# Kernel tuning notes

Hardware: AMD Instinct MI355X
Metric: run time of the kernel (lower is better)

Reference implementation:

```python
import jax, jax.numpy as jnp
import numpy as np

B, E, H, W = 8, 1024, 16, 1024
DH = E // H


def setup_inputs() -> dict:
    key = jax.random.key(0)
    ks = jax.random.split(key, 5)
    scale = E ** (-0.5)
    return {
        "x": jax.random.normal(ks[0], (3, B, E, W), dtype=jnp.float32),
        "L_Q": jax.random.normal(ks[1], (E, E), dtype=jnp.float32) * scale,
        "L_K": jax.random.normal(ks[2], (E, E), dtype=jnp.float32) * scale,
        "L_V": jax.random.normal(ks[3], (E, E), dtype=jnp.float32) * scale,
        "dense_M": jax.random.normal(ks[4], (E, E), dtype=jnp.float32) * scale,
        "dense_b": jnp.zeros((E, 1), dtype=jnp.float32),
    }


def reference(x, L_Q, L_K, L_V, dense_M, dense_b):
    # x: [3, B, E, W], channels-first sequences (dropout layers are identity in eval)
    K, Q, V = x[0], x[1], x[2]                      # each [B, E, W]
    K = jnp.einsum('ef,bfw->bew', L_K, K)
    Q = jnp.einsum('ef,bfw->bew', L_Q, Q)
    V = jnp.einsum('ef,bfw->bew', L_V, V)
    Kv = K.reshape(B, H, DH, W)
    Qv = Q.reshape(B, H, DH, W)
    Vv = V.reshape(B, H, DH, W)
    # Q_v^T @ K_v -> [B, H, Wq, Wk]
    scores = jnp.einsum('bhdq,bhdk->bhqk', Qv, Kv)
    # causal_factor = tril(-inf, diag=-1): -inf strictly below the diagonal (q > k)
    qi = jnp.arange(W)[:, None]
    ki = jnp.arange(W)[None, :]
    scores = jnp.where(qi > ki, -jnp.inf, scores)
    # softmax over the QUERY axis (-2), post-scaled by E^-0.5 (non-standard)
    attn = jax.nn.softmax(scores, axis=-2) * (E ** (-0.5))
    # V_v @ scores: contract over the query axis -> [B, H, DH, Wk]
    out = jnp.einsum('bhdq,bhqk->bhdk', Vv, attn).reshape(B, E, W)
    # dense output projection: M @ out + b (bias broadcasts over W)
    return jnp.einsum('ef,bfw->bew', dense_M, out) + dense_b
```

## Files before the change

### kernel.cpp

```cpp
#include <hip/hip_runtime.h>

typedef float  f4  __attribute__((ext_vector_type(4)));
typedef short  s8v __attribute__((ext_vector_type(8)));
typedef unsigned short u16;
typedef u16 us4 __attribute__((ext_vector_type(4)));

constexpr int En  = 1024;
constexpr int Wn  = 1024;
constexpr int Bn  = 8;
constexpr int Hn  = 16;
constexpr int DHn = 64;

__device__ inline u16 bf16rn(float x) {
    unsigned u = __float_as_uint(x);
    return (u16)((u + 0x7FFFu + ((u >> 16) & 1u)) >> 16);
}
__device__ inline float bf16tof(u16 h) { return __uint_as_float(((unsigned)h) << 16); }

#define GLD_LDS16(gp, lp) __builtin_amdgcn_global_load_lds(                      \
    (const __attribute__((address_space(1))) void*)(gp),                         \
    (__attribute__((address_space(3))) void*)(lp), 16, 0, 0)

__global__ void split_plain(const float* __restrict__ in, u16* __restrict__ hi,
                            u16* __restrict__ lo, int n4) {
    int i = blockIdx.x * blockDim.x + threadIdx.x;
    if (i >= n4) return;
    f4 v = ((const f4*)in)[i];
    us4 h, l;
    #pragma unroll
    for (int k = 0; k < 4; ++k) {
        u16 hh = bf16rn(v[k]);
        h[k] = hh;
        l[k] = bf16rn(v[k] - bf16tof(hh));
    }
    ((us4*)hi)[i] = h;
    ((us4*)lo)[i] = l;
}

__global__ void f32_to_bf16(const float* __restrict__ in, u16* __restrict__ out,
                            int n4) {
    int i = blockIdx.x * blockDim.x + threadIdx.x;
    if (i >= n4) return;
    f4 v = ((const f4*)in)[i];
    us4 o;
    #pragma unroll
    for (int k = 0; k < 4; ++k) o[k] = bf16rn(v[k]);
    ((us4*)out)[i] = o;
}

__global__ __launch_bounds__(256)
void split_t(const float* __restrict__ in, u16* __restrict__ hi,
             u16* __restrict__ lo) {
    __shared__ float T[32][33];
    const int z = blockIdx.z;
    const size_t zo = (size_t)z * En * Wn;
    const int r0 = blockIdx.y * 32, c0 = blockIdx.x * 32;
    const int t = threadIdx.x;
    const int row = t >> 3, c4 = (t & 7) << 2;

    f4 v = *(const f4*)&in[zo + (size_t)(r0 + row) * Wn + c0 + c4];
    T[row][c4 + 0] = v[0]; T[row][c4 + 1] = v[1];
    T[row][c4 + 2] = v[2]; T[row][c4 + 3] = v[3];
    __syncthreads();

    const int oc = row, r4 = c4;
    us4 h, l;
    #pragma unroll
    for (int i = 0; i < 4; ++i) {
        float x = T[r4 + i][oc];
        u16 hh = bf16rn(x);
        h[i] = hh;
        l[i] = bf16rn(x - bf16tof(hh));
    }
    *(us4*)&hi[zo + (size_t)(c0 + oc) * En + r0 + r4] = h;
    *(us4*)&lo[zo + (size_t)(c0 + oc) * En + r0 + r4] = l;
}

__global__ __launch_bounds__(256)
void qk_repack(const float* __restrict__ in, u16* __restrict__ oh,
               u16* __restrict__ ol) {
    __shared__ float T[64][65];
    const int bh = blockIdx.y, w0 = blockIdx.x * 64;
    const int t = threadIdx.x;
    const int row = t >> 2, cc = (t & 3) << 4;

    #pragma unroll
    for (int c = 0; c < 4; ++c) {
        f4 v = *(const f4*)&in[(size_t)(bh * 64 + row) * Wn + w0 + cc + c * 4];
        T[row][cc + c * 4 + 0] = v[0]; T[row][cc + c * 4 + 1] = v[1];
        T[row][cc + c * 4 + 2] = v[2]; T[row][cc + c * 4 + 3] = v[3];
    }
    __syncthreads();

    const size_t ob = ((size_t)bh * Wn + w0 + row) * 64 + cc;
    #pragma unroll
    for (int c = 0; c < 4; ++c) {
        us4 h, l;
        #pragma unroll
        for (int j = 0; j < 4; ++j) {
            float x = T[cc + c * 4 + j][row];
            u16 hh = bf16rn(x);
            h[j] = hh;
            l[j] = bf16rn(x - bf16tof(hh));
        }
        *(us4*)&oh[ob + c * 4] = h;
        *(us4*)&ol[ob + c * 4] = l;
    }
}

__global__ __launch_bounds__(256, 2)
void gemm_mfma(const u16* __restrict__ Ah,  const u16* __restrict__ Al,
               const u16* __restrict__ Bth, const u16* __restrict__ Btl,
               float* __restrict__ Y, const float* __restrict__ bias) {
    __shared__ u16 AsH[4096], AsL[4096], BsH[4096], BsL[4096];

    const int z  = blockIdx.z;
    const size_t zB = (size_t)z * Wn * En;
    const size_t zY = (size_t)z * En * Wn;
    const int e0 = blockIdx.y * 128, n0 = blockIdx.x * 128;
    const int t = threadIdx.x, lane = t & 63, wave = t >> 6;
    const int q = lane >> 4, r = lane & 15;
    const int m_off = (wave & 1) * 64, n_off = (wave >> 1) * 64;

    f4 acc[4][4];
    #pragma unroll
    for (int i = 0; i < 4; ++i)
        #pragma unroll
        for (int j = 0; j < 4; ++j) { acc[i][j][0]=0; acc[i][j][1]=0; acc[i][j][2]=0; acc[i][j][3]=0; }

    for (int kb = 0; kb < En; kb += 32) {
        __syncthreads();
        #pragma unroll
        for (int it = 0; it < 2; ++it) {
            const int id = t + 256 * it;
            const int u = id >> 3;
            const int p = (id & 7) ^ (u & 7);
            const int m = 2 * u + (p >> 2), g = p & 3;
            const size_t colA = (size_t)kb + 8 * g;
            const u16* ga_h = Ah  + (size_t)(e0 + m) * En + colA;
            const u16* ga_l = Al  + (size_t)(e0 + m) * En + colA;
            const u16* gb_h = Bth + zB + (size_t)(n0 + m) * En + colA;
            const u16* gb_l = Btl + zB + (size_t)(n0 + m) * En + colA;
            GLD_LDS16(ga_h, &AsH[id * 8]);
            GLD_LDS16(ga_l, &AsL[id * 8]);
            GLD_LDS16(gb_h, &BsH[id * 8]);
            GLD_LDS16(gb_l, &BsL[id * 8]);
        }
        __syncthreads();

        s8v aH[4], aL[4], bH[4], bL[4];
        #pragma unroll
        for (int i = 0; i < 4; ++i) {
            const int Ra = m_off + 16 * i + r;
            const int Rb = n_off + 16 * i + r;
            const int sa = ((((Ra & 1) << 2) | q) ^ ((Ra >> 1) & 7));
            const int sb = ((((Rb & 1) << 2) | q) ^ ((Rb >> 1) & 7));
            const int ai = ((Ra >> 1) * 8 + sa) * 8;
            const int bi = ((Rb >> 1) * 8 + sb) * 8;
            aH[i] = *(const s8v*)&AsH[ai];
            aL[i] = *(const s8v*)&AsL[ai];
            bH[i] = *(const s8v*)&BsH[bi];
            bL[i] = *(const s8v*)&BsL[bi];
        }
        #pragma unroll
        for (int i = 0; i < 4; ++i)
            #pragma unroll
            for (int j = 0; j < 4; ++j) {
                acc[i][j] = __builtin_amdgcn_mfma_f32_16x16x32_bf16(aH[i], bH[j], acc[i][j], 0, 0, 0);
                acc[i][j] = __builtin_amdgcn_mfma_f32_16x16x32_bf16(aH[i], bL[j], acc[i][j], 0, 0, 0);
                acc[i][j] = __builtin_amdgcn_mfma_f32_16x16x32_bf16(aL[i], bH[j], acc[i][j], 0, 0, 0);
            }
    }

    #pragma unroll
    for (int i = 0; i < 4; ++i) {
        #pragma unroll
        for (int reg = 0; reg < 4; ++reg) {
            const int e = e0 + m_off + 16 * i + q * 4 + reg;
            const float bv = bias ? bias[e] : 0.0f;
            #pragma unroll
            for (int j = 0; j < 4; ++j) {
                const int w = n0 + n_off + 16 * j + r;
                Y[zY + (size_t)e * Wn + w] = acc[i][j][reg] + bv;
            }
        }
    }
}

__global__ __launch_bounds__(256, 2)
void attn_mfma2(const u16* __restrict__ QTh, const u16* __restrict__ QTl,
                const u16* __restrict__ KTh, const u16* __restrict__ KTl,
                const u16* __restrict__ Vb,  float* __restrict__ Ao) {
    __shared__ u16 QsH[2][4096], QsL[2][4096], Vs[2][4096];
    __shared__ u16 PT[4][16][72];

    const int id   = blockIdx.x;
    const int rest = id >> 3;
    const int kb   = 15 - (rest & 15);
    const int bh   = (id & 7) + 8 * (rest >> 4);

    const int t = threadIdx.x, lane = t & 63, wave = t >> 6;
    const int r = lane & 15, quad = lane >> 4;
    const int k0 = kb * 64;
    const int kcol = k0 + wave * 16 + r;
    u16 (*pt)[72] = PT[wave];

    const size_t qkb = (size_t)bh * Wn * 64;
    const size_t vbb = (size_t)bh * 64 * Wn;

    s8v kH[2], kL[2];
    #pragma unroll
    for (int s = 0; s < 2; ++s) {
        const size_t a = qkb + (size_t)kcol * 64 + s * 32 + quad * 8;
        kH[s] = *(const s8v*)&KTh[a];
        kL[s] = *(const s8v*)&KTl[a];
    }

    f4 o[4];
    #pragma unroll
    for (int i = 0; i < 4; ++i) { o[i][0]=0; o[i][1]=0; o[i][2]=0; o[i][3]=0; }
    float m = -1e30f, l = 0.0f;

    auto stage = [&](int q0, int buf) {
        const size_t g = qkb + (size_t)q0 * 64;
        #pragma unroll
        for (int it = 0; it < 2; ++it) {
            const int c = t + it * 256;
            const int row = c >> 3;
            const int p   = (c & 7) ^ (row & 7);
            GLD_LDS16(QTh + g + (size_t)row * 64 + p * 8, &QsH[buf][c * 8]);
            GLD_LDS16(QTl + g + (size_t)row * 64 + p * 8, &QsL[buf][c * 8]);
            GLD_LDS16(Vb + vbb + (size_t)row * Wn + q0 + p * 8,
                      &Vs[buf][c * 8]);
        }
    };

    stage(0, 0);
    int buf = 0;

    for (int q0 = 0; q0 <= k0; q0 += 64) {
        __syncthreads();
        if (q0 + 64 <= k0) stage(q0 + 64, buf ^ 1);

        f4 sacc[4];
        #pragma unroll
        for (int mt = 0; mt < 4; ++mt) { sacc[mt][0]=0; sacc[mt][1]=0; sacc[mt][2]=0; sacc[mt][3]=0; }
        #pragma unroll
        for (int s = 0; s < 2; ++s) {
            const int sw = (((s * 4 + quad) ^ (r & 7)) << 3);
            #pragma unroll
            for (int mt = 0; mt < 4; ++mt) {
                const int a = (16 * mt + r) * 64 + sw;
                s8v qh = *(const s8v*)&QsH[buf][a];
                s8v ql = *(const s8v*)&QsL[buf][a];
                sacc[mt] = __builtin_amdgcn_mfma_f32_16x16x32_bf16(qh, kH[s], sacc[mt], 0, 0, 0);
                sacc[mt] = __builtin_amdgcn_mfma_f32_16x16x32_bf16(qh, kL[s], sacc[mt], 0, 0, 0);
                sacc[mt] = __builtin_amdgcn_mfma_f32_16x16x32_bf16(ql, kH[s], sacc[mt], 0, 0, 0);
            }
        }
        if (q0 == k0) {
            const int klocal = wave * 16 + r;
            #pragma unroll
            for (int mt = 0; mt < 4; ++mt)
                #pragma unroll
                for (int reg = 0; reg < 4; ++reg)
                    if (16 * mt + quad * 4 + reg > klocal) sacc[mt][reg] = -1e30f;
        }
        float tm = -1e30f;
        #pragma unroll
        for (int mt = 0; mt < 4; ++mt)
            #pragma unroll
            for (int reg = 0; reg < 4; ++reg) tm = fmaxf(tm, sacc[mt][reg]);
        tm = fmaxf(tm, __shfl_xor(tm, 16));
        tm = fmaxf(tm, __shfl_xor(tm, 32));
        const float mnew  = fmaxf(m, tm);
        const float alpha = __expf(m - mnew);
        float ps = 0.0f;
        #pragma unroll
        for (int mt = 0; mt < 4; ++mt) {
            us4 pk;
            #pragma unroll
            for (int reg = 0; reg < 4; ++reg) {
                float p = __expf(sacc[mt][reg] - mnew);
                ps += p;
                pk[reg] = bf16rn(p);
            }
            *(us4*)&pt[r][16 * mt + quad * 4] = pk;
        }
        ps += __shfl_xor(ps, 16);
        ps += __shfl_xor(ps, 32);
        l = l * alpha + ps;
        m = mnew;
        #pragma unroll
        for (int i = 0; i < 4; ++i) {
            o[i][0] *= alpha; o[i][1] *= alpha; o[i][2] *= alpha; o[i][3] *= alpha;
        }
        #pragma unroll
        for (int s = 0; s < 2; ++s) {
            const int sw = (((s * 4 + quad) ^ (r & 7)) << 3);
            s8v pf = *(const s8v*)&pt[r][s * 32 + quad * 8];
            #pragma unroll
            for (int i = 0; i < 4; ++i) {
                s8v vf = *(const s8v*)&Vs[buf][(16 * i + r) * 64 + sw];
                o[i] = __builtin_amdgcn_mfma_f32_16x16x32_bf16(vf, pf, o[i], 0, 0, 0);
            }
        }
        buf ^= 1;
    }

    const float inv = 1.0f / (l * 32.0f);
    #pragma unroll
    for (int i = 0; i < 4; ++i)
        #pragma unroll
        for (int reg = 0; reg < 4; ++reg)
            Ao[(size_t)(bh * 64 + 16 * i + quad * 4 + reg) * Wn + kcol] = o[i][reg] * inv;
}

__global__ __launch_bounds__(256, 2)
void gemm128(const float* __restrict__ L, const float* __restrict__ X,
             float* __restrict__ Y, const float* __restrict__ bias) {
    __shared__ float As[16][132];
    __shared__ float Bs[16][132];

    const int bz = blockIdx.z;
    const float* Xb = X + (size_t)bz * En * Wn;
    float*       Yb = Y + (size_t)bz * En * Wn;
    const int e0 = blockIdx.y * 128;
    const int w0 = blockIdx.x * 128;
    const int t  = threadIdx.x;
    const int tx = t & 15, ty = t >> 4;
    const int la_e = t >> 2, la_f = (t & 3) << 2;
    const int lb_f = t >> 5, lb_w = (t & 31) << 2;

    float acc[2][2][4][4] = {};

    for (int f0 = 0; f0 < En; f0 += 16) {
        f4 a0 = *(const f4*)&L [(size_t)(e0 + la_e)      * En + f0 + la_f];
        f4 a1 = *(const f4*)&L [(size_t)(e0 + la_e + 64) * En + f0 + la_f];
        f4 b0 = *(const f4*)&Xb[(size_t)(f0 + lb_f)      * Wn + w0 + lb_w];
        f4 b1 = *(const f4*)&Xb[(size_t)(f0 + lb_f + 8)  * Wn + w0 + lb_w];
        __syncthreads();
        As[la_f + 0][la_e] = a0[0]; As[la_f + 1][la_e] = a0[1];
        As[la_f + 2][la_e] = a0[2]; As[la_f + 3][la_e] = a0[3];
        As[la_f + 0][la_e + 64] = a1[0]; As[la_f + 1][la_e + 64] = a1[1];
        As[la_f + 2][la_e + 64] = a1[2]; As[la_f + 3][la_e + 64] = a1[3];
        *(f4*)&Bs[lb_f    ][lb_w] = b0;
        *(f4*)&Bs[lb_f + 8][lb_w] = b1;
        __syncthreads();
        #pragma unroll
        for (int kk = 0; kk < 16; ++kk) {
            f4 av0 = *(f4*)&As[kk][ty * 4];
            f4 av1 = *(f4*)&As[kk][ty * 4 + 64];
            f4 bv0 = *(f4*)&Bs[kk][tx * 4];
            f4 bv1 = *(f4*)&Bs[kk][tx * 4 + 64];
            #pragma unroll
            for (int i = 0; i < 4; ++i)
                #pragma unroll
                for (int j = 0; j < 4; ++j) {
                    acc[0][0][i][j] = fmaf(av0[i], bv0[j], acc[0][0][i][j]);
                    acc[0][1][i][j] = fmaf(av0[i], bv1[j], acc[0][1][i][j]);
                    acc[1][0][i][j] = fmaf(av1[i], bv0[j], acc[1][0][i][j]);
                    acc[1][1][i][j] = fmaf(av1[i], bv1[j], acc[1][1][i][j]);
                }
        }
    }

    #pragma unroll
    for (int eh = 0; eh < 2; ++eh)
        #pragma unroll
        for (int i = 0; i < 4; ++i) {
            const int e = e0 + eh * 64 + ty * 4 + i;
            const float bv = bias ? bias[e] : 0.0f;
            #pragma unroll
            for (int wh = 0; wh < 2; ++wh) {
                f4 v;
                #pragma unroll
                for (int j = 0; j < 4; ++j) v[j] = acc[eh][wh][i][j] + bv;
                *(f4*)&Yb[(size_t)e * Wn + w0 + wh * 64 + tx * 4] = v;
            }
        }
}

__global__ __launch_bounds__(256, 2)
void attn64(const float* __restrict__ Qg, const float* __restrict__ Kg,
            const float* __restrict__ Vg, float* __restrict__ Og) {
    __shared__ float Ks[64][68];
    __shared__ float QP[64][68];
    __shared__ float Vt[64][68];
    __shared__ float mArr[64], lArr[64], alphaArr[64];
    __shared__ float red[4][64];

    const int kb = blockIdx.x, h = blockIdx.y, b = blockIdx.z;
    const size_t base = ((size_t)b * En + (size_t)h * DHn) * Wn;
    const float* Qp = Qg + base;
    const float* Kp = Kg + base;
    const float* Vp = Vg + base;
    float*       Op = Og + base;

    const int t  = threadIdx.x;
    const int tx = t & 15, ty = t >> 4;
    const int lr = t >> 4;
    const int lc = (t & 15) << 2;
    const int k0 = kb * 64;
    const int kc = t & 63, qg = t >> 6;

    #pragma unroll
    for (int r = 0; r < 4; ++r)
        *(f4*)&Ks[lr + r * 16][lc] =
            *(const f4*)&Kp[(size_t)(lr + r * 16) * Wn + k0 + lc];
    if (t < 64) { mArr[t] = -1e30f; lArr[t] = 0.0f; }
    float acc[4][4] = {};
    __syncthreads();

    for (int q0 = 0; q0 <= k0; q0 += 64) {
        #pragma unroll
        for (int r = 0; r < 4; ++r) {
            const int d = lr + r * 16;
            f4 qv = *(const f4*)&Qp[(size_t)d * Wn + q0 + lc];
            f4 vv = *(const f4*)&Vp[(size_t)d * Wn + q0 + lc];
            *(f4*)&QP[d][lc] = qv;
            Vt[lc + 0][d] = vv[0]; Vt[lc + 1][d] = vv[1];
            Vt[lc + 2][d] = vv[2]; Vt[lc + 3][d] = vv[3];
        }
        __syncthreads();

        float s[4][4] = {};
        #pragma unroll 4
        for (int d = 0; d < 64; ++d) {
            f4 kv = *(f4*)&Ks[d][tx * 4];
            f4 q2 = *(f4*)&QP[d][ty * 4];
            #pragma unroll
            for (int i = 0; i < 4; ++i)
                #pragma unroll
                for (int j = 0; j < 4; ++j)
                    s[i][j] = fmaf(q2[i], kv[j], s[i][j]);
        }
        if (q0 == k0) {
            #pragma unroll
            for (int i = 0; i < 4; ++i)
                #pragma unroll
                for (int j = 0; j < 4; ++j)
                    if (ty * 4 + i > tx * 4 + j) s[i][j] = -1e30f;
        }
        __syncthreads();
        #pragma unroll
        for (int i = 0; i < 4; ++i) {
            f4 v;
            #pragma unroll
            for (int j = 0; j < 4; ++j) v[j] = s[i][j];
            *(f4*)&QP[ty * 4 + i][tx * 4] = v;
        }
        __syncthreads();

        float sv[16];
        float lm = -1e30f;
        #pragma unroll
        for (int r = 0; r < 16; ++r) {
            sv[r] = QP[qg * 16 + r][kc];
            lm = fmaxf(lm, sv[r]);
        }
        red[qg][kc] = lm;
        __syncthreads();
        const float mt    = fmaxf(fmaxf(red[0][kc], red[1][kc]),
                                  fmaxf(red[2][kc], red[3][kc]));
        const float mprev = mArr[kc];
        const float mnew  = fmaxf(mprev, mt);
        float psum = 0.0f;
        #pragma unroll
        for (int r = 0; r < 16; ++r) {
            const float p = __expf(sv[r] - mnew);
            psum += p;
            QP[qg * 16 + r][kc] = p;
        }
        __syncthreads();
        red[qg][kc] = psum;
        __syncthreads();
        if (qg == 0) {
            const float alpha = __expf(mprev - mnew);
            lArr[kc] = lArr[kc] * alpha +
                       (red[0][kc] + red[1][kc] + red[2][kc] + red[3][kc]);
            mArr[kc]     = mnew;
            alphaArr[kc] = alpha;
        }
        __syncthreads();

        f4 al = *(f4*)&alphaArr[tx * 4];
        #pragma unroll
        for (int i = 0; i < 4; ++i)
            #pragma unroll
            for (int j = 0; j < 4; ++j)
                acc[i][j] *= al[j];
        #pragma unroll 4
        for (int q = 0; q < 64; ++q) {
            f4 pv = *(f4*)&QP[q][tx * 4];
            f4 v2 = *(f4*)&Vt[q][ty * 4];
            #pragma unroll
            for (int i = 0; i < 4; ++i)
                #pragma unroll
                for (int j = 0; j < 4; ++j)
                    acc[i][j] = fmaf(v2[i], pv[j], acc[i][j]);
        }
        __syncthreads();
    }

    f4 linv = *(f4*)&lArr[tx * 4];
    #pragma unroll
    for (int j = 0; j < 4; ++j) linv[j] = 1.0f / (linv[j] * 32.0f);
    #pragma unroll
    for (int i = 0; i < 4; ++i) {
        f4 v;
        #pragma unroll
        for (int j = 0; j < 4; ++j) v[j] = acc[i][j] * linv[j];
        *(f4*)&Op[(size_t)(ty * 4 + i) * Wn + k0 + tx * 4] = v;
    }
}

extern "C" void kernel_launch(void* const* d_in, const int* in_sizes, int n_in,
                              void* d_out, int out_size, void* d_ws, size_t ws_size,
                              hipStream_t stream) {
    const float* x    = (const float*)d_in[0];
    const float* L_Q  = (const float*)d_in[1];
    const float* L_K  = (const float*)d_in[2];
    const float* L_V  = (const float*)d_in[3];
    const float* M    = (const float*)d_in[4];
    const float* bias = (const float*)d_in[5];
    float* out = (float*)d_out;

    const size_t mat   = (size_t)Bn * En * Wn;
    const size_t matB  = mat * 4;
    const size_t lmatB = (size_t)En * En * 2;
    const size_t need  = 8 * lmatB + 5 * matB;

    if (ws_size >= need) {
        char* w = (char*)d_ws;
        u16*  Lsp = (u16*)w;
        char* XT  = w + 8 * lmatB;
        char* RC  = XT + matB;
        char* RD  = RC + matB;
        char* RE  = RD + matB;
        char* RF  = RE + matB;

        u16* LKh = Lsp + 0 * (lmatB / 2); u16* LKl = Lsp + 1 * (lmatB / 2);
        u16* LQh = Lsp + 2 * (lmatB / 2); u16* LQl = Lsp + 3 * (lmatB / 2);
        u16* LVh = Lsp + 4 * (lmatB / 2); u16* LVl = Lsp + 5 * (lmatB / 2);
        u16* Mh  = Lsp + 6 * (lmatB / 2); u16* Ml  = Lsp + 7 * (lmatB / 2);

        u16* XT_H = (u16*)XT;          u16* XT_L = (u16*)(XT + matB / 2);
        float* Kp = (float*)RC;
        u16* KT_h = (u16*)RF;          u16* KT_l = (u16*)(RF + matB / 2);
        float* Qp = (float*)RD;
        u16* QT_h = (u16*)RC;          u16* QT_l = (u16*)(RC + matB / 2);
        float* Vp = (float*)RE;
        u16* Vb   = (u16*)RD;
        float* Ao = (float*)RE;

        const int n4L = En * En / 4;
        hipLaunchKernelGGL(split_plain, dim3(n4L / 256), dim3(256), 0, stream, L_K, LKh, LKl, n4L);
        hipLaunchKernelGGL(split_plain, dim3(n4L / 256), dim3(256), 0, stream, L_Q, LQh, LQl, n4L);
        hipLaunchKernelGGL(split_plain, dim3(n4L / 256), dim3(256), 0, stream, L_V, LVh, LVl, n4L);
        hipLaunchKernelGGL(split_plain, dim3(n4L / 256), dim3(256), 0, stream, M,   Mh,  Ml,  n4L);

        dim3 gt(Wn / 32, En / 32, Bn), bt(256);
        dim3 gg(Wn / 128, En / 128, Bn), bg(256);
        dim3 gr(Wn / 64, Bn * Hn);

        hipLaunchKernelGGL(split_t, gt, bt, 0, stream, x + 0 * mat, XT_H, XT_L);
        hipLaunchKernelGGL(gemm_mfma, gg, bg, 0, stream, LKh, LKl, XT_H, XT_L, Kp, (const float*)nullptr);
        hipLaunchKernelGGL(qk_repack, gr, dim3(256), 0, stream, Kp, KT_h, KT_l);
        hipLaunchKernelGGL(split_t, gt, bt, 0, stream, x + 1 * mat, XT_H, XT_L);
        hipLaunchKernelGGL(gemm_mfma, gg, bg, 0, stream, LQh, LQl, XT_H, XT_L, Qp, (const float*)nullptr);
        hipLaunchKernelGGL(qk_repack, gr, dim3(256), 0, stream, Qp, QT_h, QT_l);
        hipLaunchKernelGGL(split_t, gt, bt, 0, stream, x + 2 * mat, XT_H, XT_L);
        hipLaunchKernelGGL(gemm_mfma, gg, bg, 0, stream, LVh, LVl, XT_H, XT_L, Vp, (const float*)nullptr);
        hipLaunchKernelGGL(f32_to_bf16, dim3((int)(mat / 4 / 256)), dim3(256), 0, stream, Vp, Vb, (int)(mat / 4));

        hipLaunchKernelGGL(attn_mfma2, dim3(2048), dim3(256), 0, stream,
                           QT_h, QT_l, KT_h, KT_l, Vb, Ao);

        hipLaunchKernelGGL(split_t, gt, bt, 0, stream, Ao, XT_H, XT_L);
        hipLaunchKernelGGL(gemm_mfma, gg, bg, 0, stream, Mh, Ml, XT_H, XT_L, out, bias);
    } else {
        float* ws = (float*)d_ws;
        float* Kp = ws;
        float* Qp = ws + mat;
        float* Vp = ws + 2 * mat;
        float* Ao = ws + 3 * mat;

        dim3 gg(Wn / 128, En / 128, Bn), blk(256);
        hipLaunchKernelGGL(gemm128, gg, blk, 0, stream, L_K, x + 0 * mat, Kp, (const float*)nullptr);
        hipLaunchKernelGGL(gemm128, gg, blk, 0, stream, L_Q, x + 1 * mat, Qp, (const float*)nullptr);
        hipLaunchKernelGGL(gemm128, gg, blk, 0, stream, L_V, x + 2 * mat, Vp, (const float*)nullptr);

        dim3 ga(Wn / 64, Hn, Bn);
        hipLaunchKernelGGL(attn64, ga, blk, 0, stream, Qp, Kp, Vp, Ao);

        hipLaunchKernelGGL(gemm128, gg, blk, 0, stream, M, Ao, out, bias);
    }
}
```

Before: 505.3 us.

## Fuse bf16 split/repack into GEMM epilogues and attention output, register-staged attention

```diff
diff --git a/kernel.cpp b/kernel.cpp
--- a/kernel.cpp
+++ b/kernel.cpp
@@ -35,17 +35,6 @@
     }
     ((us4*)hi)[i] = h;
     ((us4*)lo)[i] = l;
-}
-
-__global__ void f32_to_bf16(const float* __restrict__ in, u16* __restrict__ out,
-                            int n4) {
-    int i = blockIdx.x * blockDim.x + threadIdx.x;
-    if (i >= n4) return;
-    f4 v = ((const f4*)in)[i];
-    us4 o;
-    #pragma unroll
-    for (int k = 0; k < 4; ++k) o[k] = bf16rn(v[k]);
-    ((us4*)out)[i] = o;
 }
 
 __global__ __launch_bounds__(256)
@@ -76,47 +65,16 @@
     *(us4*)&lo[zo + (size_t)(c0 + oc) * En + r0 + r4] = l;
 }
 
-__global__ __launch_bounds__(256)
-void qk_repack(const float* __restrict__ in, u16* __restrict__ oh,
-               u16* __restrict__ ol) {
-    __shared__ float T[64][65];
-    const int bh = blockIdx.y, w0 = blockIdx.x * 64;
-    const int t = threadIdx.x;
-    const int row = t >> 2, cc = (t & 3) << 4;
-
-    #pragma unroll
-    for (int c = 0; c < 4; ++c) {
-        f4 v = *(const f4*)&in[(size_t)(bh * 64 + row) * Wn + w0 + cc + c * 4];
-        T[row][cc + c * 4 + 0] = v[0]; T[row][cc + c * 4 + 1] = v[1];
-        T[row][cc + c * 4 + 2] = v[2]; T[row][cc + c * 4 + 3] = v[3];
-    }
-    __syncthreads();
-
-    const size_t ob = ((size_t)bh * Wn + w0 + row) * 64 + cc;
-    #pragma unroll
-    for (int c = 0; c < 4; ++c) {
-        us4 h, l;
-        #pragma unroll
-        for (int j = 0; j < 4; ++j) {
-            float x = T[cc + c * 4 + j][row];
-            u16 hh = bf16rn(x);
-            h[j] = hh;
-            l[j] = bf16rn(x - bf16tof(hh));
-        }
-        *(us4*)&oh[ob + c * 4] = h;
-        *(us4*)&ol[ob + c * 4] = l;
-    }
-}
-
+template<int MODE>
 __global__ __launch_bounds__(256, 2)
 void gemm_mfma(const u16* __restrict__ Ah,  const u16* __restrict__ Al,
                const u16* __restrict__ Bth, const u16* __restrict__ Btl,
-               float* __restrict__ Y, const float* __restrict__ bias) {
+               float* __restrict__ Yf, u16* __restrict__ Yh, u16* __restrict__ Yl,
+               const float* __restrict__ bias) {
     __shared__ u16 AsH[4096], AsL[4096], BsH[4096], BsL[4096];
 
     const int z  = blockIdx.z;
     const size_t zB = (size_t)z * Wn * En;
-    const size_t zY = (size_t)z * En * Wn;
     const int e0 = blockIdx.y * 128, n0 = blockIdx.x * 128;
     const int t = threadIdx.x, lane = t & 63, wave = t >> 6;
     const int q = lane >> 4, r = lane & 15;
@@ -172,26 +130,70 @@
             }
     }
 
-    #pragma unroll
-    for (int i = 0; i < 4; ++i) {
-        #pragma unroll
-        for (int reg = 0; reg < 4; ++reg) {
-            const int e = e0 + m_off + 16 * i + q * 4 + reg;
-            const float bv = bias ? bias[e] : 0.0f;
+    if constexpr (MODE == 0) {
+        const size_t zY = (size_t)z * En * Wn;
+        #pragma unroll
+        for (int i = 0; i < 4; ++i) {
+            #pragma unroll
+            for (int reg = 0; reg < 4; ++reg) {
+                const int e = e0 + m_off + 16 * i + q * 4 + reg;
+                const float bv = bias ? bias[e] : 0.0f;
+                #pragma unroll
+                for (int j = 0; j < 4; ++j) {
+                    const int w = n0 + n_off + 16 * j + r;
+                    Yf[zY + (size_t)e * Wn + w] = acc[i][j][reg] + bv;
+                }
+            }
+        }
+    }
+    if constexpr (MODE == 1) {
+        #pragma unroll
+        for (int i = 0; i < 4; ++i) {
+            const int e_base = e0 + m_off + 16 * i + q * 4;
+            const int bh_e = z * Hn + (e_base >> 6);
+            const int d0 = e_base & 63;
             #pragma unroll
             for (int j = 0; j < 4; ++j) {
                 const int w = n0 + n_off + 16 * j + r;
-                Y[zY + (size_t)e * Wn + w] = acc[i][j][reg] + bv;
-            }
-        }
-    }
-}
-
-__global__ __launch_bounds__(256, 2)
-void attn_mfma2(const u16* __restrict__ QTh, const u16* __restrict__ QTl,
+                us4 h, l;
+                #pragma unroll
+                for (int reg = 0; reg < 4; ++reg) {
+                    float x = acc[i][j][reg];
+                    u16 hh = bf16rn(x);
+                    h[reg] = hh;
+                    l[reg] = bf16rn(x - bf16tof(hh));
+                }
+                const size_t o = ((size_t)bh_e * Wn + w) * 64 + d0;
+                *(us4*)&Yh[o] = h;
+                *(us4*)&Yl[o] = l;
+            }
+        }
+    }
+    if constexpr (MODE == 2) {
+        #pragma unroll
+        for (int i = 0; i < 4; ++i) {
+            #pragma unroll
+            for (int reg = 0; reg < 4; ++reg) {
+                const int e = e0 + m_off + 16 * i + q * 4 + reg;
+                const int bh_e = z * Hn + (e >> 6);
+                const int d = e & 63;
+                const size_t ro = ((size_t)bh_e * 64 + d) * Wn;
+                #pragma unroll
+                for (int j = 0; j < 4; ++j) {
+                    const int w = n0 + n_off + 16 * j + r;
+                    Yh[ro + w] = bf16rn(acc[i][j][reg]);
+                }
+            }
+        }
+    }
+}
+
+__global__ __launch_bounds__(256, 3)
+void attn_mfma3(const u16* __restrict__ QTh, const u16* __restrict__ QTl,
                 const u16* __restrict__ KTh, const u16* __restrict__ KTl,
-                const u16* __restrict__ Vb,  float* __restrict__ Ao) {
-    __shared__ u16 QsH[2][4096], QsL[2][4096], Vs[2][4096];
+                const u16* __restrict__ Vb,  u16* __restrict__ AoTh,
+                u16* __restrict__ AoTl) {
+    __shared__ u16 QsH[4096], QsL[4096], Vs[4096];
     __shared__ u16 PT[4][16][72];
 
     const int id   = blockIdx.x;
@@ -221,27 +223,28 @@
     for (int i = 0; i < 4; ++i) { o[i][0]=0; o[i][1]=0; o[i][2]=0; o[i][3]=0; }
     float m = -1e30f, l = 0.0f;
 
-    auto stage = [&](int q0, int buf) {
+    const int c0 = t,       row0 = c0 >> 3, p0 = (c0 & 7) ^ (row0 & 7);
+    const int c1 = t + 256, row1 = c1 >> 3, p1 = (c1 & 7) ^ (row1 & 7);
+
+    s8v Aqh0, Aqh1, Aql0, Aql1, Av0, Av1;
+    s8v Bqh0, Bqh1, Bql0, Bql1, Bv0, Bv1;
+
+    auto ld = [&](int q0, s8v& qh0, s8v& qh1, s8v& ql0, s8v& ql1,
+                  s8v& v0, s8v& v1) {
         const size_t g = qkb + (size_t)q0 * 64;
-        #pragma unroll
-        for (int it = 0; it < 2; ++it) {
-            const int c = t + it * 256;
-            const int row = c >> 3;
-            const int p   = (c & 7) ^ (row & 7);
-            GLD_LDS16(QTh + g + (size_t)row * 64 + p * 8, &QsH[buf][c * 8]);
-            GLD_LDS16(QTl + g + (size_t)row * 64 + p * 8, &QsL[buf][c * 8]);
-            GLD_LDS16(Vb + vbb + (size_t)row * Wn + q0 + p * 8,
-                      &Vs[buf][c * 8]);
-        }
+        qh0 = *(const s8v*)&QTh[g + (size_t)row0 * 64 + p0 * 8];
+        ql0 = *(const s8v*)&QTl[g + (size_t)row0 * 64 + p0 * 8];
+        v0  = *(const s8v*)&Vb[vbb + (size_t)row0 * Wn + q0 + p0 * 8];
+        qh1 = *(const s8v*)&QTh[g + (size_t)row1 * 64 + p1 * 8];
+        ql1 = *(const s8v*)&QTl[g + (size_t)row1 * 64 + p1 * 8];
+        v1  = *(const s8v*)&Vb[vbb + (size_t)row1 * Wn + q0 + p1 * 8];
     };
-
-    stage(0, 0);
-    int buf = 0;
-
-    for (int q0 = 0; q0 <= k0; q0 += 64) {
-        __syncthreads();
-        if (q0 + 64 <= k0) stage(q0 + 64, buf ^ 1);
-
+    auto wr = [&](s8v& qh0, s8v& qh1, s8v& ql0, s8v& ql1, s8v& v0, s8v& v1) {
+        *(s8v*)&QsH[c0 * 8] = qh0; *(s8v*)&QsL[c0 * 8] = ql0; *(s8v*)&Vs[c0 * 8] = v0;
+        *(s8v*)&QsH[c1 * 8] = qh1; *(s8v*)&QsL[c1 * 8] = ql1; *(s8v*)&Vs[c1 * 8] = v1;
+    };
+
+    auto compute = [&](int q0) {
         f4 sacc[4];
         #pragma unroll
         for (int mt = 0; mt < 4; ++mt) { sacc[mt][0]=0; sacc[mt][1]=0; sacc[mt][2]=0; sacc[mt][3]=0; }
@@ -251,8 +254,8 @@
             #pragma unroll
             for (int mt = 0; mt < 4; ++mt) {
                 const int a = (16 * mt + r) * 64 + sw;
-                s8v qh = *(const s8v*)&QsH[buf][a];
-                s8v ql = *(const s8v*)&QsL[buf][a];
+                s8v qh = *(const s8v*)&QsH[a];
+                s8v ql = *(const s8v*)&QsL[a];
                 sacc[mt] = __builtin_amdgcn_mfma_f32_16x16x32_bf16(qh, kH[s], sacc[mt], 0, 0, 0);
                 sacc[mt] = __builtin_amdgcn_mfma_f32_16x16x32_bf16(qh, kL[s], sacc[mt], 0, 0, 0);
                 sacc[mt] = __builtin_amdgcn_mfma_f32_16x16x32_bf16(ql, kH[s], sacc[mt], 0, 0, 0);
@@ -301,19 +304,47 @@
             s8v pf = *(const s8v*)&pt[r][s * 32 + quad * 8];
             #pragma unroll
             for (int i = 0; i < 4; ++i) {
-                s8v vf = *(const s8v*)&Vs[buf][(16 * i + r) * 64 + sw];
+                s8v vf = *(const s8v*)&Vs[(16 * i + r) * 64 + sw];
                 o[i] = __builtin_amdgcn_mfma_f32_16x16x32_bf16(vf, pf, o[i], 0, 0, 0);
             }
         }
-        buf ^= 1;
+    };
+
+    ld(0, Aqh0, Aqh1, Aql0, Aql1, Av0, Av1);
+    int q0 = 0;
+    for (;;) {
+        __syncthreads();
+        wr(Aqh0, Aqh1, Aql0, Aql1, Av0, Av1);
+        __syncthreads();
+        if (q0 + 64 <= k0) ld(q0 + 64, Bqh0, Bqh1, Bql0, Bql1, Bv0, Bv1);
+        compute(q0);
+        q0 += 64;
+        if (q0 > k0) break;
+        __syncthreads();
+        wr(Bqh0, Bqh1, Bql0, Bql1, Bv0, Bv1);
+        __syncthreads();
+        if (q0 + 64 <= k0) ld(q0 + 64, Aqh0, Aqh1, Aql0, Aql1, Av0, Av1);
+        compute(q0);
+        q0 += 64;
+        if (q0 > k0) break;
     }
 
     const float inv = 1.0f / (l * 32.0f);
-    #pragma unroll
-    for (int i = 0; i < 4; ++i)
-        #pragma unroll
-        for (int reg = 0; reg < 4; ++reg)
-            Ao[(size_t)(bh * 64 + 16 * i + quad * 4 + reg) * Wn + kcol] = o[i][reg] * inv;
+    const size_t ob0 = (size_t)(bh >> 4) * ((size_t)Wn * En) +
+                       (size_t)kcol * En + (bh & 15) * 64 + quad * 4;
+    #pragma unroll
+    for (int i = 0; i < 4; ++i) {
+        us4 h, lo4;
+        #pragma unroll
+        for (int reg = 0; reg < 4; ++reg) {
+            float x = o[i][reg] * inv;
+            u16 hh = bf16rn(x);
+            h[reg] = hh;
+            lo4[reg] = bf16rn(x - bf16tof(hh));
+        }
+        *(us4*)&AoTh[ob0 + 16 * i] = h;
+        *(us4*)&AoTl[ob0 + 16 * i] = lo4;
+    }
 }
 
 __global__ __launch_bounds__(256, 2)
@@ -529,30 +560,27 @@
     const size_t mat   = (size_t)Bn * En * Wn;
     const size_t matB  = mat * 4;
     const size_t lmatB = (size_t)En * En * 2;
-    const size_t need  = 8 * lmatB + 5 * matB;
+    const size_t need  = 8 * lmatB + 4 * matB + matB / 2 + matB;
 
     if (ws_size >= need) {
         char* w = (char*)d_ws;
         u16*  Lsp = (u16*)w;
         char* XT  = w + 8 * lmatB;
-        char* RC  = XT + matB;
-        char* RD  = RC + matB;
-        char* RE  = RD + matB;
-        char* RF  = RE + matB;
+        char* R1  = XT + matB;
+        char* R2  = R1 + matB;
+        char* R3  = R2 + matB;
+        char* R4  = R3 + matB / 2;
 
         u16* LKh = Lsp + 0 * (lmatB / 2); u16* LKl = Lsp + 1 * (lmatB / 2);
         u16* LQh = Lsp + 2 * (lmatB / 2); u16* LQl = Lsp + 3 * (lmatB / 2);
         u16* LVh = Lsp + 4 * (lmatB / 2); u16* LVl = Lsp + 5 * (lmatB / 2);
         u16* Mh  = Lsp + 6 * (lmatB / 2); u16* Ml  = Lsp + 7 * (lmatB / 2);
 
-        u16* XT_H = (u16*)XT;          u16* XT_L = (u16*)(XT + matB / 2);
-        float* Kp = (float*)RC;
-        u16* KT_h = (u16*)RF;          u16* KT_l = (u16*)(RF + matB / 2);
-        float* Qp = (float*)RD;
-        u16* QT_h = (u16*)RC;          u16* QT_l = (u16*)(RC + matB / 2);
-        float* Vp = (float*)RE;
-        u16* Vb   = (u16*)RD;
-        float* Ao = (float*)RE;
+        u16* XT_H = (u16*)XT;  u16* XT_L = (u16*)(XT + matB / 2);
+        u16* KT_h = (u16*)R1;  u16* KT_l = (u16*)(R1 + matB / 2);
+        u16* QT_h = (u16*)R2;  u16* QT_l = (u16*)(R2 + matB / 2);
+        u16* Vb   = (u16*)R3;
+        u16* AoTh = (u16*)R4;  u16* AoTl = (u16*)(R4 + matB / 2);
 
         const int n4L = En * En / 4;
         hipLaunchKernelGGL(split_plain, dim3(n4L / 256), dim3(256), 0, stream, L_K, LKh, LKl, n4L);
@@ -562,23 +590,22 @@
 
         dim3 gt(Wn / 32, En / 32, Bn), bt(256);
         dim3 gg(Wn / 128, En / 128, Bn), bg(256);
-        dim3 gr(Wn / 64, Bn * Hn);
 
         hipLaunchKernelGGL(split_t, gt, bt, 0, stream, x + 0 * mat, XT_H, XT_L);
-        hipLaunchKernelGGL(gemm_mfma, gg, bg, 0, stream, LKh, LKl, XT_H, XT_L, Kp, (const float*)nullptr);
-        hipLaunchKernelGGL(qk_repack, gr, dim3(256), 0, stream, Kp, KT_h, KT_l);
+        hipLaunchKernelGGL(HIP_KERNEL_NAME(gemm_mfma<1>), gg, bg, 0, stream,
+                           LKh, LKl, XT_H, XT_L, (float*)nullptr, KT_h, KT_l, (const float*)nullptr);
         hipLaunchKernelGGL(split_t, gt, bt, 0, stream, x + 1 * mat, XT_H, XT_L);
-        hipLaunchKernelGGL(gemm_mfma, gg, bg, 0, stream, LQh, LQl, XT_H, XT_L, Qp, (const float*)nullptr);
-        hipLaunchKernelGGL(qk_repack, gr, dim3(256), 0, stream, Qp, QT_h, QT_l);
+        hipLaunchKernelGGL(HIP_KERNEL_NAME(gemm_mfma<1>), gg, bg, 0, stream,
+                           LQh, LQl, XT_H, XT_L, (float*)nullptr, QT_h, QT_l, (const float*)nullptr);
         hipLaunchKernelGGL(split_t, gt, bt, 0, stream, x + 2 * mat, XT_H, XT_L);
-        hipLaunchKernelGGL(gemm_mfma, gg, bg, 0, stream, LVh, LVl, XT_H, XT_L, Vp, (const float*)nullptr);
-        hipLaunchKernelGGL(f32_to_bf16, dim3((int)(mat / 4 / 256)), dim3(256), 0, stream, Vp, Vb, (int)(mat / 4));
-
-        hipLaunchKernelGGL(attn_mfma2, dim3(2048), dim3(256), 0, stream,
-                           QT_h, QT_l, KT_h, KT_l, Vb, Ao);
-
-        hipLaunchKernelGGL(split_t, gt, bt, 0, stream, Ao, XT_H, XT_L);
-        hipLaunchKernelGGL(gemm_mfma, gg, bg, 0, stream, Mh, Ml, XT_H, XT_L, out, bias);
+        hipLaunchKernelGGL(HIP_KERNEL_NAME(gemm_mfma<2>), gg, bg, 0, stream,
+                           LVh, LVl, XT_H, XT_L, (float*)nullptr, Vb, (u16*)nullptr, (const float*)nullptr);
+
+        hipLaunchKernelGGL(attn_mfma3, dim3(2048), dim3(256), 0, stream,
+                           QT_h, QT_l, KT_h, KT_l, Vb, AoTh, AoTl);
+
+        hipLaunchKernelGGL(HIP_KERNEL_NAME(gemm_mfma<0>), gg, bg, 0, stream,
+                           Mh, Ml, AoTh, AoTl, out, (u16*)nullptr, (u16*)nullptr, bias);
     } else {
         float* ws = (float*)d_ws;
         float* Kp = ws;
```

After: 465.4 us. 1.09x faster.
